# Optimization experiments

Measured on AMD Instinct MI355X. Metric: run time of the kernel, lower is better.

The kernel has to match this reference:

```python
import jax, jax.numpy as jnp
import numpy as np

B, D, H = 64, 512, 8
EPS = 1e-8


def setup_inputs() -> dict:
    key = jax.random.key(0)
    k1, k2, k3 = jax.random.split(key, 3)
    x = jax.random.normal(k1, (B, D), dtype=jnp.float32)
    # alphas/betas: one scalar per (head, transform); columns = (query, key, value)
    alphas = jax.random.uniform(k2, (H, 3), dtype=jnp.float32)
    betas = jax.random.uniform(k3, (H, 3), dtype=jnp.float32)
    return {"x": x, "alphas": alphas, "betas": betas}


def reference(x, alphas, betas):
    # x: [B, D]; alphas, betas: [H, 3] (query, key, value scalar affine params per head)
    d = x.shape[-1]
    # qkv[h, t, b, d] = alphas[h, t] * x[b, d] + betas[h, t]  (ones vector -> plain bias)
    qkv = alphas[:, :, None, None] * x[None, None, :, :] + betas[:, :, None, None]  # [H,3,B,D]
    q, k, v = qkv[:, 0], qkv[:, 1], qkv[:, 2]  # each [H, B, D]
    # diff[h,b,i,j] = |q[h,b,j] - k[h,b,i]|  (row i = key feature, col j = query feature)
    diff = jnp.abs(q[:, :, None, :] - k[:, :, :, None]) + EPS  # [H, B, D, D]
    sim = jax.nn.softmax(1.0 / diff, axis=-1) / jnp.sqrt(jnp.float32(d))
    # attended[h,b,i] = sum_j sim[h,b,i,j] * v[h,b,j]  (batched matvec)
    attended = jnp.einsum("hbij,hbj->hbi", sim, v)  # [H, B, D]
    return x + attended.sum(axis=0)
```

## Files before the change

### kernel.cpp

```cpp
#include <hip/hip_runtime.h>
#include <math.h>

#define BB 64
#define DD 512
#define HH 8
#define EPS 1e-8f

__device__ float g_xsorted[BB][DD];
__device__ int   g_perm[BB][DD];

__device__ __forceinline__ float fast_rcp(float d) {
    return __builtin_amdgcn_rcpf(d);
}

__global__ __launch_bounds__(DD) void sort_kernel(const float* __restrict__ x)
{
    const int b   = blockIdx.x;
    const int tid = threadIdx.x;
    __shared__ float sv[DD];
    __shared__ int   si[DD];
    sv[tid] = x[b * DD + tid];
    si[tid] = tid;
    __syncthreads();
    for (int k = 2; k <= DD; k <<= 1) {
        for (int j = k >> 1; j > 0; j >>= 1) {
            const int ixj = tid ^ j;
            if (ixj > tid) {
                const bool up = ((tid & k) == 0);
                float v0 = sv[tid], v1 = sv[ixj];
                bool sw = up ? (v0 > v1) : (v0 < v1);
                if (sw) {
                    int i0 = si[tid], i1 = si[ixj];
                    sv[tid] = v1; sv[ixj] = v0;
                    si[tid] = i1; si[ixj] = i0;
                }
            }
            __syncthreads();
        }
    }
    g_xsorted[b][tid] = sv[tid];
    g_perm[b][tid]    = si[tid];
}

__global__ __launch_bounds__(512, 8) void flattn_kernel(
    const float* __restrict__ x,
    const float* __restrict__ alphas,
    const float* __restrict__ betas,
    float* __restrict__ out)
{
    const int b  = blockIdx.x;
    const int ic = blockIdx.y;
    const int h  = blockIdx.z;

    __shared__ float xs[DD];
    __shared__ float xss[DD];
    __shared__ float mind_sh[2][256];
    __shared__ float ss_sh[256];
    __shared__ float sx_sh[256];

    const int tid  = threadIdx.x;
    const int ii   = tid & 255;
    const int jc   = tid >> 8;
    const int rank = ic * 256 + ii;

    const float a0 = alphas[h * 3 + 0];
    const float a1 = alphas[h * 3 + 1];
    const float a2 = alphas[h * 3 + 2];
    const float b0 = betas[h * 3 + 0];
    const float b1 = betas[h * 3 + 1];
    const float b2 = betas[h * 3 + 2];

    xs[tid]  = x[b * DD + tid];
    xss[tid] = g_xsorted[b][tid];
    __syncthreads();

    const float xi = xss[rank];
    const float c  = b0 - fmaf(a1, xi, b1);

    const float ra0 = fast_rcp(a0);
    const float u   = -c * ra0;

    int pos = 0;
    #pragma unroll
    for (int s = 512; s > 0; s >>= 1) {
        int p = pos + s;
        float v = xss[(p <= 512 ? p : 512) - 1];
        pos = (p <= 512 && v < u) ? p : pos;
    }
    float mind_hat = 3.0e38f;
    #pragma unroll
    for (int q = -2; q <= 1; ++q) {
        int cidx = pos + q;
        if (cidx >= 0 && cidx < DD)
            mind_hat = fminf(mind_hat, fabsf(fmaf(a0, xss[cidx], c)));
    }
    const float mhat = fast_rcp(mind_hat + EPS);

    const float th  = fast_rcp(fmaxf(mhat - 30.0f, 1e-30f));
    const float tha = fmaf(th * 1.0001f, ra0, 1e-6f);
    const float xlo = u - tha;
    const float xhi = u + tha;

    int lo = 0, hi = 0;
    #pragma unroll
    for (int s = 512; s > 0; s >>= 1) {
        int pl = lo + s, ph = hi + s;
        float vl = xss[(pl <= 512 ? pl : 512) - 1];
        float vh = xss[(ph <= 512 ? ph : 512) - 1];
        lo = (pl <= 512 && vl <  xlo) ? pl : lo;
        hi = (ph <= 512 && vh <= xhi) ? ph : hi;
    }
    lo = max(lo - 2, 0);
    hi = min(hi + 2, DD);
    const int len = hi - lo;

    const bool lane_peaked = (a0 > 1e-6f) && (mhat > 60.0f) && (len <= 64);
    const bool peaked = __all(lane_peaked);

    const float log2e = 1.4426950408889634f;

    float md = 3.0e38f;
    int wl = 0, wh = 0;
    const int j0 = jc * 256;
    if (peaked) {
        const int mid = lo + ((len + 1) >> 1);
        wl = jc ? mid : lo;
        wh = jc ? hi  : mid;
        for (int k = wl; k < wh; ++k)
            md = fminf(md, fabsf(fmaf(a0, xss[k], c)));
    } else {
        #pragma unroll 4
        for (int j = j0; j < j0 + 256; j += 4) {
            float4 x4 = *(const float4*)&xs[j];
            md = fminf(md, fabsf(fmaf(a0, x4.x, c)));
            md = fminf(md, fabsf(fmaf(a0, x4.y, c)));
            md = fminf(md, fabsf(fmaf(a0, x4.z, c)));
            md = fminf(md, fabsf(fmaf(a0, x4.w, c)));
        }
    }
    mind_sh[jc][ii] = md;
    __syncthreads();

    const float mind  = fminf(mind_sh[0][ii], mind_sh[1][ii]);
    const float m     = fast_rcp(mind + EPS);
    const float negml = -m * log2e;

    float ss = 0.0f, sx = 0.0f;
    if (peaked) {
        for (int k = wl; k < wh; ++k) {
            float xv = xss[k];
            float t  = fmaf(a0, xv, c);
            float r  = fast_rcp(fabsf(t) + EPS);
            float s  = __builtin_amdgcn_exp2f(fmaf(r, log2e, negml));
            ss += s; sx = fmaf(s, xv, sx);
        }
    } else {
        #pragma unroll 2
        for (int j = j0; j < j0 + 256; j += 4) {
            float4 x4 = *(const float4*)&xs[j];
            {
                float t = fmaf(a0, x4.x, c);
                float r = fast_rcp(fabsf(t) + EPS);
                float s = __builtin_amdgcn_exp2f(fmaf(r, log2e, negml));
                ss += s; sx = fmaf(s, x4.x, sx);
            }
            {
                float t = fmaf(a0, x4.y, c);
                float r = fast_rcp(fabsf(t) + EPS);
                float s = __builtin_amdgcn_exp2f(fmaf(r, log2e, negml));
                ss += s; sx = fmaf(s, x4.y, sx);
            }
            {
                float t = fmaf(a0, x4.z, c);
                float r = fast_rcp(fabsf(t) + EPS);
                float s = __builtin_amdgcn_exp2f(fmaf(r, log2e, negml));
                ss += s; sx = fmaf(s, x4.z, sx);
            }
            {
                float t = fmaf(a0, x4.w, c);
                float r = fast_rcp(fabsf(t) + EPS);
                float s = __builtin_amdgcn_exp2f(fmaf(r, log2e, negml));
                ss += s; sx = fmaf(s, x4.w, sx);
            }
        }
    }

    if (jc == 1) { ss_sh[ii] = ss; sx_sh[ii] = sx; }
    __syncthreads();
    if (jc == 0) {
        ss += ss_sh[ii];
        sx += sx_sh[ii];
        const float scale = 0.04419417382415922f;
        float sv  = fmaf(a2, sx, b2 * ss);
        float att = sv * fast_rcp(ss) * scale;
        if (h == 0) att += xi;
        const int i_orig = g_perm[b][rank];
        atomicAdd(&out[b * DD + i_orig], att);
    }
}

extern "C" void kernel_launch(void* const* d_in, const int* in_sizes, int n_in,
                              void* d_out, int out_size, void* d_ws, size_t ws_size,
                              hipStream_t stream) {
    const float* x      = (const float*)d_in[0];
    const float* alphas = (const float*)d_in[1];
    const float* betas  = (const float*)d_in[2];
    float* out = (float*)d_out;

    hipMemsetAsync(out, 0, (size_t)out_size * sizeof(float), stream);

    sort_kernel<<<dim3(BB), dim3(DD), 0, stream>>>(x);

    dim3 grid(BB, 2, HH);
    dim3 block(512);
    flattn_kernel<<<grid, block, 0, stream>>>(x, alphas, betas, out);
}
```

Measured before the change: 98.69 us.

## Replace bitonic sort with rank-counting sort, fold output zeroing, relax peaked thresholds

Swaps the shared-memory bitonic sort, with its many barriers, for a stable rank-by-counting sort in which each thread counts smaller elements and scatters its value and index directly. The output memset is folded into the sort kernel, which removes one launch. The peaked fast-path thresholds are loosened (mhat > 45, window up to 128) so more warps take the windowed path instead of the full 256-element scan. The looser cutoff could let the truncated window drop softmax mass that still matters for accuracy.

```diff
diff --git a/kernel.cpp b/kernel.cpp
--- a/kernel.cpp
+++ b/kernel.cpp
@@ -13,33 +13,28 @@
     return __builtin_amdgcn_rcpf(d);
 }
 
-__global__ __launch_bounds__(DD) void sort_kernel(const float* __restrict__ x)
+__global__ __launch_bounds__(DD) void sort_kernel(const float* __restrict__ x,
+                                                  float* __restrict__ out)
 {
     const int b   = blockIdx.x;
     const int tid = threadIdx.x;
     __shared__ float sv[DD];
-    __shared__ int   si[DD];
-    sv[tid] = x[b * DD + tid];
-    si[tid] = tid;
-    __syncthreads();
-    for (int k = 2; k <= DD; k <<= 1) {
-        for (int j = k >> 1; j > 0; j >>= 1) {
-            const int ixj = tid ^ j;
-            if (ixj > tid) {
-                const bool up = ((tid & k) == 0);
-                float v0 = sv[tid], v1 = sv[ixj];
-                bool sw = up ? (v0 > v1) : (v0 < v1);
-                if (sw) {
-                    int i0 = si[tid], i1 = si[ixj];
-                    sv[tid] = v1; sv[ixj] = v0;
-                    si[tid] = i1; si[ixj] = i0;
-                }
-            }
-            __syncthreads();
-        }
-    }
-    g_xsorted[b][tid] = sv[tid];
-    g_perm[b][tid]    = si[tid];
+    const float xi = x[b * DD + tid];
+    sv[tid] = xi;
+    out[b * DD + tid] = 0.0f;
+    __syncthreads();
+
+    int cnt = 0;
+    #pragma unroll 4
+    for (int j = 0; j < DD; j += 4) {
+        float4 v = *(const float4*)&sv[j];
+        cnt += (int)((v.x < xi) | ((v.x == xi) & ((j + 0) < tid)));
+        cnt += (int)((v.y < xi) | ((v.y == xi) & ((j + 1) < tid)));
+        cnt += (int)((v.z < xi) | ((v.z == xi) & ((j + 2) < tid)));
+        cnt += (int)((v.w < xi) | ((v.w == xi) & ((j + 3) < tid)));
+    }
+    g_xsorted[b][cnt] = xi;
+    g_perm[b][cnt]    = tid;
 }
 
 __global__ __launch_bounds__(512, 8) void flattn_kernel(
@@ -114,7 +109,7 @@
     hi = min(hi + 2, DD);
     const int len = hi - lo;
 
-    const bool lane_peaked = (a0 > 1e-6f) && (mhat > 60.0f) && (len <= 64);
+    const bool lane_peaked = (a0 > 1e-6f) && (mhat > 45.0f) && (len <= 128);
     const bool peaked = __all(lane_peaked);
 
     const float log2e = 1.4426950408889634f;
@@ -207,9 +202,7 @@
     const float* betas  = (const float*)d_in[2];
     float* out = (float*)d_out;
 
-    hipMemsetAsync(out, 0, (size_t)out_size * sizeof(float), stream);
-
-    sort_kernel<<<dim3(BB), dim3(DD), 0, stream>>>(x);
+    sort_kernel<<<dim3(BB), dim3(DD), 0, stream>>>(x, out);
 
     dim3 grid(BB, 2, HH);
     dim3 block(512);
```

Measured after the change: 102.7 us. 1.04x slower.
